# Performance work log

Measured on AMD Instinct MI355X. Metric: run time of the kernel, lower is better.

Reference implementation:

```python
import jax, jax.numpy as jnp
import numpy as np

N_NODES = 100000


def setup_inputs() -> dict:
    key = jax.random.key(0)
    k1, k2, k3, k4 = jax.random.split(key, 4)
    E = 1600000
    D_IN, D_OUT = 256, 256
    feat = jax.random.normal(k1, (N_NODES, D_IN), dtype=jnp.float32)
    src = jax.random.randint(k2, (E,), 0, N_NODES, dtype=jnp.int32)
    dst = jax.random.randint(k3, (E,), 0, N_NODES, dtype=jnp.int32)
    # xavier_uniform-like init for weight
    limit = np.sqrt(6.0 / (D_IN + D_OUT)).astype(np.float32)
    weight = jax.random.uniform(k4, (D_IN, D_OUT), dtype=jnp.float32,
                                minval=-limit, maxval=limit)
    bias = jnp.zeros((D_OUT,), dtype=jnp.float32)
    return {"feat": feat, "src": src, "dst": dst, "weight": weight, "bias": bias}


def reference(feat, src, dst, weight, bias):
    ones = jnp.ones(src.shape[0], dtype=feat.dtype)
    # out_degrees: number of outgoing edges per node (src counts)
    out_deg = jax.ops.segment_sum(ones, src, num_segments=N_NODES)
    # in_degrees: number of incoming edges per node (dst counts)
    in_deg = jax.ops.segment_sum(ones, dst, num_segments=N_NODES)
    # norm == 'both': pre-scale by out_deg^-0.5
    pre = jnp.power(jnp.clip(out_deg, 1.0), -0.5)[:, None]  # [N,1]
    h = feat * pre
    # message passing: copy_src + sum over incoming edges (SpMM)
    agg = jax.ops.segment_sum(h[src], dst, num_segments=N_NODES)  # [N, D_in]
    # dense projection
    rst = agg @ weight  # [N, D_out]
    # post-scale by in_deg^-0.5
    post = jnp.power(jnp.clip(in_deg, 1.0), -0.5)[:, None]
    rst = rst * post + bias
    return rst
```

## Files before the change

### kernel.cpp

```cpp
#include <hip/hip_runtime.h>
#include <hip/hip_bf16.h>
#include <stdint.h>


using short8  = __attribute__((ext_vector_type(8))) short;
using floatx4 = __attribute__((ext_vector_type(4))) float;

static __device__ __forceinline__ unsigned short f32_to_bf16(float f) {
    unsigned int u = __float_as_uint(f);
    u += 0x7FFFu + ((u >> 16) & 1u);
    return (unsigned short)(u >> 16);
}
static __device__ __forceinline__ float bf2f(unsigned short u) {
    return __uint_as_float((unsigned int)u << 16);
}

__global__ void k_deg(const int* __restrict__ src, const int* __restrict__ dst,
                      int E, int* __restrict__ outc, int* __restrict__ inc) {
    int i = blockIdx.x * blockDim.x + threadIdx.x;
    int stride = gridDim.x * blockDim.x;
    for (; i < E; i += stride) {
        atomicAdd(&outc[src[i]], 1);
        atomicAdd(&inc[dst[i]], 1);
    }
}

__global__ void k_off(const int* __restrict__ inc, int N, int* __restrict__ total,
                      int* __restrict__ start, int* __restrict__ cursor) {
    __shared__ int ss[256];
    __shared__ int sbase;
    int t = threadIdx.x;
    int i = blockIdx.x * 256 + t;
    int d = (i < N) ? inc[i] : 0;
    int v = d;
    ss[t] = v;
    __syncthreads();
    for (int off = 1; off < 256; off <<= 1) {
        int u = (t >= off) ? ss[t - off] : 0;
        __syncthreads();
        v += u;
        ss[t] = v;
        __syncthreads();
    }
    if (t == 255) sbase = atomicAdd(total, v);
    __syncthreads();
    if (i < N) {
        int b = sbase + (v - d);
        start[i] = b;
        cursor[i] = b;
    }
}

__global__ void k_fill(const int* __restrict__ src, const int* __restrict__ dst,
                       int E, int* __restrict__ cursor, int* __restrict__ eidx) {
    int i = blockIdx.x * blockDim.x + threadIdx.x;
    int stride = gridDim.x * blockDim.x;
    for (; i < E; i += stride) {
        int p = atomicAdd(&cursor[dst[i]], 1);
        eidx[p] = src[i];
    }
}

__global__ void k_wt(const float* __restrict__ W, unsigned short* __restrict__ WT) {
    int i = blockIdx.x * blockDim.x + threadIdx.x;
    int n = i >> 8, k = i & 255;
    WT[n * 256 + k] = f32_to_bf16(W[(size_t)k * 256 + n]);
}

__global__ void k_hb(const float* __restrict__ feat, const int* __restrict__ outc,
                     int N, unsigned short* __restrict__ h) {
    int node = blockIdx.x * 4 + (threadIdx.x >> 6);
    if (node >= N) return;
    int lane = threadIdx.x & 63;
    float p = rsqrtf((float)max(outc[node], 1));
    float4 v = *(const float4*)(feat + (size_t)node * 256 + lane * 4);
    ushort4 u;
    u.x = f32_to_bf16(v.x * p);
    u.y = f32_to_bf16(v.y * p);
    u.z = f32_to_bf16(v.z * p);
    u.w = f32_to_bf16(v.w * p);
    *(ushort4*)(h + (size_t)node * 256 + lane * 4) = u;
}

__global__ void __launch_bounds__(256)
k_gemm(unsigned short* h , const unsigned short* __restrict__ WT,
       int N) {
    int wave = blockIdx.x * 4 + (threadIdx.x >> 6);
    int m0 = wave * 16;
    if (m0 >= N) return;
    int lane = threadIdx.x & 63;
    int r = lane & 15;
    int g = lane >> 4;

    floatx4 acc[16];
#pragma unroll
    for (int n = 0; n < 16; ++n) acc[n] = (floatx4){0.f, 0.f, 0.f, 0.f};

#pragma unroll
    for (int k = 0; k < 8; ++k) {
        short8 a = *(const short8*)(h + (size_t)(m0 + r) * 256 + k * 32 + g * 8);
#pragma unroll
        for (int n = 0; n < 16; ++n) {
            short8 b = *(const short8*)(WT + (size_t)(n * 16 + r) * 256 + k * 32 + g * 8);
            acc[n] = __builtin_amdgcn_mfma_f32_16x16x32_bf16(a, b, acc[n], 0, 0, 0);
        }
    }

#pragma unroll
    for (int n = 0; n < 16; ++n) {
        int c = n * 16 + r;
#pragma unroll
        for (int i = 0; i < 4; ++i) {
            int row = m0 + g * 4 + i;
            h[(size_t)row * 256 + c] = f32_to_bf16(acc[n][i]);
        }
    }
}

__global__ void k_agg(const unsigned short* __restrict__ z,
                      const int* __restrict__ start, const int* __restrict__ inc,
                      const int* __restrict__ eidx, const float* __restrict__ bias,
                      int N, float* __restrict__ out) {
    int node = blockIdx.x * 4 + (threadIdx.x >> 6);
    if (node >= N) return;
    int lane = threadIdx.x & 63;
    int deg = inc[node];
    const int* ep = eidx + start[node];

    float a0 = 0.f, a1 = 0.f, a2 = 0.f, a3 = 0.f;
    float b0 = 0.f, b1 = 0.f, b2 = 0.f, b3 = 0.f;
    float c0 = 0.f, c1 = 0.f, c2 = 0.f, c3 = 0.f;
    float d0 = 0.f, d1 = 0.f, d2 = 0.f, d3 = 0.f;
    int e = 0;
    for (; e + 3 < deg; e += 4) {
        int sA = ep[e], sB = ep[e + 1], sC = ep[e + 2], sD = ep[e + 3];
        ushort4 vA = *(const ushort4*)(z + (size_t)sA * 256 + lane * 4);
        ushort4 vB = *(const ushort4*)(z + (size_t)sB * 256 + lane * 4);
        ushort4 vC = *(const ushort4*)(z + (size_t)sC * 256 + lane * 4);
        ushort4 vD = *(const ushort4*)(z + (size_t)sD * 256 + lane * 4);
        a0 += bf2f(vA.x); a1 += bf2f(vA.y); a2 += bf2f(vA.z); a3 += bf2f(vA.w);
        b0 += bf2f(vB.x); b1 += bf2f(vB.y); b2 += bf2f(vB.z); b3 += bf2f(vB.w);
        c0 += bf2f(vC.x); c1 += bf2f(vC.y); c2 += bf2f(vC.z); c3 += bf2f(vC.w);
        d0 += bf2f(vD.x); d1 += bf2f(vD.y); d2 += bf2f(vD.z); d3 += bf2f(vD.w);
    }
    for (; e < deg; ++e) {
        int s = ep[e];
        ushort4 v = *(const ushort4*)(z + (size_t)s * 256 + lane * 4);
        a0 += bf2f(v.x); a1 += bf2f(v.y); a2 += bf2f(v.z); a3 += bf2f(v.w);
    }
    a0 += b0 + c0 + d0;
    a1 += b1 + c1 + d1;
    a2 += b2 + c2 + d2;
    a3 += b3 + c3 + d3;

    float post = rsqrtf((float)max(deg, 1));
    float4 bs = *(const float4*)(bias + lane * 4);
    float4 o;
    o.x = a0 * post + bs.x;
    o.y = a1 * post + bs.y;
    o.z = a2 * post + bs.z;
    o.w = a3 * post + bs.w;
    *(float4*)(out + (size_t)node * 256 + lane * 4) = o;
}

extern "C" void kernel_launch(void* const* d_in, const int* in_sizes, int n_in,
                              void* d_out, int out_size, void* d_ws, size_t ws_size,
                              hipStream_t stream) {
    const float* feat = (const float*)d_in[0];
    const int*   src  = (const int*)d_in[1];
    const int*   dst  = (const int*)d_in[2];
    const float* W    = (const float*)d_in[3];
    const float* bias = (const float*)d_in[4];
    float* out = (float*)d_out;

    const int D = 256;
    int N = in_sizes[0] / D;
    int E = in_sizes[1];

    char* ws = (char*)d_ws;
    size_t off = 0;
    auto alloc = [&](size_t bytes) -> void* {
        void* p = ws + off;
        off += (bytes + 255) & ~(size_t)255;
        return p;
    };
    int*            cnt    = (int*)alloc(((size_t)2 * N + 64) * sizeof(int));
    int*            outc   = cnt;
    int*            inc    = cnt + N;
    int*            total  = cnt + 2 * N;
    int*            start  = (int*)alloc((size_t)N * sizeof(int));
    int*            cursor = (int*)alloc((size_t)N * sizeof(int));
    int*            eidx   = (int*)alloc((size_t)E * sizeof(int));
    unsigned short* h      = (unsigned short*)alloc((size_t)N * D * sizeof(unsigned short));
    unsigned short* WT     = (unsigned short*)alloc((size_t)D * D * sizeof(unsigned short));
    (void)ws_size;

    hipMemsetAsync(cnt, 0, ((size_t)2 * N + 64) * sizeof(int), stream);

    k_deg<<<1024, 256, 0, stream>>>(src, dst, E, outc, inc);
    k_off<<<(N + 255) / 256, 256, 0, stream>>>(inc, N, total, start, cursor);
    k_fill<<<1024, 256, 0, stream>>>(src, dst, E, cursor, eidx);
    k_wt<<<(D * D) / 256, 256, 0, stream>>>(W, WT);
    k_hb<<<(N + 3) / 4, 256, 0, stream>>>(feat, outc, N, h);
    k_gemm<<<(N / 16 + 3) / 4, 256, 0, stream>>>(h, WT, N);
    k_agg<<<(N + 3) / 4, 256, 0, stream>>>(h, start, inc, eidx, bias, N, out);
}
```

Before: 680.5 us.

## Fuse prescale into GEMM, drop start array, widen aggregation loads

Removes the separate prescale/bf16 conversion kernel by loading fp32 features directly in the GEMM, scaling by the out-degree rsqrt and converting to bf16 in registers. This avoids writing and rereading an intermediate bf16 feature buffer. It also derives CSR start offsets from the post-fill cursor, which removes the start array. The aggregation kernel now has each half-wave gather a different edge with 16-byte loads and combines the halves with a cross-lane shuffle. Edge kernels switch from grid-stride loops to one thread per edge.

```diff
diff --git a/kernel.cpp b/kernel.cpp
--- a/kernel.cpp
+++ b/kernel.cpp
@@ -5,6 +5,7 @@
 
 using short8  = __attribute__((ext_vector_type(8))) short;
 using floatx4 = __attribute__((ext_vector_type(4))) float;
+using ushort8 = __attribute__((ext_vector_type(8))) unsigned short;
 
 static __device__ __forceinline__ unsigned short f32_to_bf16(float f) {
     unsigned int u = __float_as_uint(f);
@@ -18,15 +19,14 @@
 __global__ void k_deg(const int* __restrict__ src, const int* __restrict__ dst,
                       int E, int* __restrict__ outc, int* __restrict__ inc) {
     int i = blockIdx.x * blockDim.x + threadIdx.x;
-    int stride = gridDim.x * blockDim.x;
-    for (; i < E; i += stride) {
+    if (i < E) {
         atomicAdd(&outc[src[i]], 1);
         atomicAdd(&inc[dst[i]], 1);
     }
 }
 
 __global__ void k_off(const int* __restrict__ inc, int N, int* __restrict__ total,
-                      int* __restrict__ start, int* __restrict__ cursor) {
+                      int* __restrict__ cursor) {
     __shared__ int ss[256];
     __shared__ int sbase;
     int t = threadIdx.x;
@@ -44,18 +44,13 @@
     }
     if (t == 255) sbase = atomicAdd(total, v);
     __syncthreads();
-    if (i < N) {
-        int b = sbase + (v - d);
-        start[i] = b;
-        cursor[i] = b;
-    }
+    if (i < N) cursor[i] = sbase + (v - d);
 }
 
 __global__ void k_fill(const int* __restrict__ src, const int* __restrict__ dst,
                        int E, int* __restrict__ cursor, int* __restrict__ eidx) {
     int i = blockIdx.x * blockDim.x + threadIdx.x;
-    int stride = gridDim.x * blockDim.x;
-    for (; i < E; i += stride) {
+    if (i < E) {
         int p = atomicAdd(&cursor[dst[i]], 1);
         eidx[p] = src[i];
     }
@@ -67,24 +62,10 @@
     WT[n * 256 + k] = f32_to_bf16(W[(size_t)k * 256 + n]);
 }
 
-__global__ void k_hb(const float* __restrict__ feat, const int* __restrict__ outc,
-                     int N, unsigned short* __restrict__ h) {
-    int node = blockIdx.x * 4 + (threadIdx.x >> 6);
-    if (node >= N) return;
-    int lane = threadIdx.x & 63;
-    float p = rsqrtf((float)max(outc[node], 1));
-    float4 v = *(const float4*)(feat + (size_t)node * 256 + lane * 4);
-    ushort4 u;
-    u.x = f32_to_bf16(v.x * p);
-    u.y = f32_to_bf16(v.y * p);
-    u.z = f32_to_bf16(v.z * p);
-    u.w = f32_to_bf16(v.w * p);
-    *(ushort4*)(h + (size_t)node * 256 + lane * 4) = u;
-}
-
 __global__ void __launch_bounds__(256)
-k_gemm(unsigned short* h , const unsigned short* __restrict__ WT,
-       int N) {
+k_gemm(const float* __restrict__ feat, const int* __restrict__ outc,
+       const unsigned short* __restrict__ WT, int N,
+       unsigned short* __restrict__ z) {
     int wave = blockIdx.x * 4 + (threadIdx.x >> 6);
     int m0 = wave * 16;
     if (m0 >= N) return;
@@ -92,13 +73,27 @@
     int r = lane & 15;
     int g = lane >> 4;
 
+    int row = m0 + r;
+    float p = rsqrtf((float)max(outc[row], 1));
+    const float4* arow = (const float4*)(feat + (size_t)row * 256);
+
     floatx4 acc[16];
 #pragma unroll
     for (int n = 0; n < 16; ++n) acc[n] = (floatx4){0.f, 0.f, 0.f, 0.f};
 
 #pragma unroll
     for (int k = 0; k < 8; ++k) {
-        short8 a = *(const short8*)(h + (size_t)(m0 + r) * 256 + k * 32 + g * 8);
+        float4 v0 = arow[k * 8 + g * 2];
+        float4 v1 = arow[k * 8 + g * 2 + 1];
+        short8 a;
+        a[0] = (short)f32_to_bf16(v0.x * p);
+        a[1] = (short)f32_to_bf16(v0.y * p);
+        a[2] = (short)f32_to_bf16(v0.z * p);
+        a[3] = (short)f32_to_bf16(v0.w * p);
+        a[4] = (short)f32_to_bf16(v1.x * p);
+        a[5] = (short)f32_to_bf16(v1.y * p);
+        a[6] = (short)f32_to_bf16(v1.z * p);
+        a[7] = (short)f32_to_bf16(v1.w * p);
 #pragma unroll
         for (int n = 0; n < 16; ++n) {
             short8 b = *(const short8*)(WT + (size_t)(n * 16 + r) * 256 + k * 32 + g * 8);
@@ -111,56 +106,53 @@
         int c = n * 16 + r;
 #pragma unroll
         for (int i = 0; i < 4; ++i) {
-            int row = m0 + g * 4 + i;
-            h[(size_t)row * 256 + c] = f32_to_bf16(acc[n][i]);
+            int rw = m0 + g * 4 + i;
+            z[(size_t)rw * 256 + c] = f32_to_bf16(acc[n][i]);
         }
     }
 }
 
 __global__ void k_agg(const unsigned short* __restrict__ z,
-                      const int* __restrict__ start, const int* __restrict__ inc,
+                      const int* __restrict__ cursor, const int* __restrict__ inc,
                       const int* __restrict__ eidx, const float* __restrict__ bias,
                       int N, float* __restrict__ out) {
     int node = blockIdx.x * 4 + (threadIdx.x >> 6);
     if (node >= N) return;
     int lane = threadIdx.x & 63;
+    int half = lane >> 5;
+    int l = lane & 31;
     int deg = inc[node];
-    const int* ep = eidx + start[node];
+    const int* ep = eidx + (cursor[node] - deg);
 
-    float a0 = 0.f, a1 = 0.f, a2 = 0.f, a3 = 0.f;
-    float b0 = 0.f, b1 = 0.f, b2 = 0.f, b3 = 0.f;
-    float c0 = 0.f, c1 = 0.f, c2 = 0.f, c3 = 0.f;
-    float d0 = 0.f, d1 = 0.f, d2 = 0.f, d3 = 0.f;
+    float acc[8];
+#pragma unroll
+    for (int j = 0; j < 8; ++j) acc[j] = 0.f;
+
     int e = 0;
-    for (; e + 3 < deg; e += 4) {
-        int sA = ep[e], sB = ep[e + 1], sC = ep[e + 2], sD = ep[e + 3];
-        ushort4 vA = *(const ushort4*)(z + (size_t)sA * 256 + lane * 4);
-        ushort4 vB = *(const ushort4*)(z + (size_t)sB * 256 + lane * 4);
-        ushort4 vC = *(const ushort4*)(z + (size_t)sC * 256 + lane * 4);
-        ushort4 vD = *(const ushort4*)(z + (size_t)sD * 256 + lane * 4);
-        a0 += bf2f(vA.x); a1 += bf2f(vA.y); a2 += bf2f(vA.z); a3 += bf2f(vA.w);
-        b0 += bf2f(vB.x); b1 += bf2f(vB.y); b2 += bf2f(vB.z); b3 += bf2f(vB.w);
-        c0 += bf2f(vC.x); c1 += bf2f(vC.y); c2 += bf2f(vC.z); c3 += bf2f(vC.w);
-        d0 += bf2f(vD.x); d1 += bf2f(vD.y); d2 += bf2f(vD.z); d3 += bf2f(vD.w);
+    for (; e + 1 < deg; e += 2) {
+        int s = ep[e + half];
+        ushort8 v = *(const ushort8*)(z + (size_t)s * 256 + l * 8);
+#pragma unroll
+        for (int j = 0; j < 8; ++j) acc[j] += bf2f(v[j]);
     }
-    for (; e < deg; ++e) {
+    if (e < deg && half == 0) {
         int s = ep[e];
-        ushort4 v = *(const ushort4*)(z + (size_t)s * 256 + lane * 4);
-        a0 += bf2f(v.x); a1 += bf2f(v.y); a2 += bf2f(v.z); a3 += bf2f(v.w);
+        ushort8 v = *(const ushort8*)(z + (size_t)s * 256 + l * 8);
+#pragma unroll
+        for (int j = 0; j < 8; ++j) acc[j] += bf2f(v[j]);
     }
-    a0 += b0 + c0 + d0;
-    a1 += b1 + c1 + d1;
-    a2 += b2 + c2 + d2;
-    a3 += b3 + c3 + d3;
+#pragma unroll
+    for (int j = 0; j < 8; ++j) acc[j] += __shfl_xor(acc[j], 32);
 
     float post = rsqrtf((float)max(deg, 1));
-    float4 bs = *(const float4*)(bias + lane * 4);
+    int c0 = l * 8 + half * 4;
+    float4 bs = *(const float4*)(bias + c0);
     float4 o;
-    o.x = a0 * post + bs.x;
-    o.y = a1 * post + bs.y;
-    o.z = a2 * post + bs.z;
-    o.w = a3 * post + bs.w;
-    *(float4*)(out + (size_t)node * 256 + lane * 4) = o;
+    o.x = acc[half * 4 + 0] * post + bs.x;
+    o.y = acc[half * 4 + 1] * post + bs.y;
+    o.z = acc[half * 4 + 2] * post + bs.z;
+    o.w = acc[half * 4 + 3] * post + bs.w;
+    *(float4*)(out + (size_t)node * 256 + c0) = o;
 }
 
 extern "C" void kernel_launch(void* const* d_in, const int* in_sizes, int n_in,
@@ -188,20 +180,18 @@
     int*            outc   = cnt;
     int*            inc    = cnt + N;
     int*            total  = cnt + 2 * N;
-    int*            start  = (int*)alloc((size_t)N * sizeof(int));
     int*            cursor = (int*)alloc((size_t)N * sizeof(int));
     int*            eidx   = (int*)alloc((size_t)E * sizeof(int));
-    unsigned short* h      = (unsigned short*)alloc((size_t)N * D * sizeof(unsigned short));
+    unsigned short* z      = (unsigned short*)alloc((size_t)N * D * sizeof(unsigned short));
     unsigned short* WT     = (unsigned short*)alloc((size_t)D * D * sizeof(unsigned short));
     (void)ws_size;
 
     hipMemsetAsync(cnt, 0, ((size_t)2 * N + 64) * sizeof(int), stream);
 
-    k_deg<<<1024, 256, 0, stream>>>(src, dst, E, outc, inc);
-    k_off<<<(N + 255) / 256, 256, 0, stream>>>(inc, N, total, start, cursor);
-    k_fill<<<1024, 256, 0, stream>>>(src, dst, E, cursor, eidx);
-    k_wt<<<(D * D) / 256, 256, 0, stream>>>(W, WT);
-    k_hb<<<(N + 3) / 4, 256, 0, stream>>>(feat, outc, N, h);
-    k_gemm<<<(N / 16 + 3) / 4, 256, 0, stream>>>(h, WT, N);
-    k_agg<<<(N + 3) / 4, 256, 0, stream>>>(h, start, inc, eidx, bias, N, out);
+    k_deg <<<(E + 255) / 256, 256, 0, stream>>>(src, dst, E, outc, inc);
+    k_off <<<(N + 255) / 256, 256, 0, stream>>>(inc, N, total, cursor);
+    k_fill<<<(E + 255) / 256, 256, 0, stream>>>(src, dst, E, cursor, eidx);
+    k_wt  <<<(D * D) / 256, 256, 0, stream>>>(W, WT);
+    k_gemm<<<(N / 16 + 3) / 4, 256, 0, stream>>>(feat, outc, WT, N, z);
+    k_agg <<<(N + 3) / 4, 256, 0, stream>>>(z, cursor, inc, eidx, bias, N, out);
 }
```

Measured after the change: 653.4 us. 4.0% less time.
